# Performance work log

Hardware: AMD Instinct MI355X
Metric: run time of the kernel (lower is better)

The kernel has to match this reference:

```python
import jax, jax.numpy as jnp
import numpy as np


def setup_inputs() -> dict:
    key = jax.random.key(0)
    k1, k2, k3 = jax.random.split(key, 3)
    B, H, W, D, K = 16, 32, 32, 128, 32
    x = jax.random.normal(k1, (B, H, W, D), dtype=jnp.float32)
    std = 1.0 / (K * D) ** 0.5
    codewords = jax.random.uniform(k2, (K, D), minval=-std, maxval=std, dtype=jnp.float32)
    scale = jax.random.uniform(k3, (K,), minval=-1.0, maxval=0.0, dtype=jnp.float32)
    return {"x": x, "codewords": codewords, "scale": scale}


def reference(x, codewords, scale):
    B, H, W, D = x.shape
    K = codewords.shape[0]
    X = x.reshape(B, H * W, D)                      # [B, N, D]
    # scaled squared distances: s_k * ||x_n - c_k||^2 via expansion (no BNKD tensor)
    x2 = jnp.sum(X * X, axis=-1, keepdims=True)     # [B, N, 1]
    c2 = jnp.sum(codewords * codewords, axis=-1)    # [K]
    xc = jnp.einsum('bnd,kd->bnk', X, codewords)    # [B, N, K]
    SL = scale[None, None, :] * (x2 - 2.0 * xc + c2[None, None, :])
    A = jax.nn.softmax(SL, axis=2)                  # assignment weights [B, N, K]
    # E_bk = sum_n A_bnk * (x_bn - c_k)
    E = jnp.einsum('bnk,bnd->bkd', A, X) - jnp.sum(A, axis=1)[:, :, None] * codewords[None]
    return E
```

## Files before the change

kernel.cpp:

```cpp
#include <hip/hip_runtime.h>


typedef __attribute__((ext_vector_type(8))) short bf16x8;
typedef __attribute__((ext_vector_type(16))) float f32x16;

constexpr int XBS = 136;
constexpr int AST = 72;

__device__ __forceinline__ unsigned short f2bf(float f) {
    unsigned u = __float_as_uint(f);
    u += 0x7fffu + ((u >> 16) & 1u);
    return (unsigned short)(u >> 16);
}
__device__ __forceinline__ float bf2f(unsigned short h) {
    return __uint_as_float((unsigned)h << 16);
}

__global__ __launch_bounds__(256)
void enc_partial(const float* __restrict__ x, const float* __restrict__ cw,
                 const float* __restrict__ scale, unsigned short* __restrict__ ws)
{
    __shared__ unsigned short xb_s[64 * XBS];
    __shared__ unsigned short cb_s[32 * XBS];
    __shared__ unsigned short At_s[32 * AST];
    __shared__ float x2_s[64], c2_s[32];
    __shared__ float asum_s[4 * 32];
    __shared__ float asumf_s[32];

    const int tid = threadIdx.x;
    const int b   = blockIdx.x >> 4;
    const int s   = blockIdx.x & 15;
    const int lc  = tid & 31;
    const int lh  = (tid >> 5) & 1;
    const int w   = tid >> 6;
    const int g   = w >> 1;
    const int p   = w & 1;

    const float4* xg4 = (const float4*)(x + (size_t)(b * 1024 + s * 64) * 128);
    const float4* cg4 = (const float4*)cw;

#pragma unroll
    for (int i = 0; i < 8; ++i) {
        const int f   = tid + 256 * i;
        const int row = 8 * i + (tid >> 5);
        const int col = tid & 31;
        float4 vx = xg4[f];
        short4 hx = { (short)f2bf(vx.x), (short)f2bf(vx.y),
                      (short)f2bf(vx.z), (short)f2bf(vx.w) };
        *(short4*)&xb_s[row * XBS + col * 4] = hx;
        float sx = vx.x * vx.x + vx.y * vx.y + vx.z * vx.z + vx.w * vx.w;
#pragma unroll
        for (int m = 16; m >= 1; m >>= 1) sx += __shfl_xor(sx, m);
        if (col == 0) x2_s[row] = sx;
    }
#pragma unroll
    for (int i = 0; i < 4; ++i) {
        const int f   = tid + 256 * i;
        const int row = 8 * i + (tid >> 5);
        const int col = tid & 31;
        float4 vc = cg4[f];
        short4 hc = { (short)f2bf(vc.x), (short)f2bf(vc.y),
                      (short)f2bf(vc.z), (short)f2bf(vc.w) };
        *(short4*)&cb_s[row * XBS + col * 4] = hc;
        float sc = vc.x * vc.x + vc.y * vc.y + vc.z * vc.z + vc.w * vc.w;
#pragma unroll
        for (int m = 16; m >= 1; m >>= 1) sc += __shfl_xor(sc, m);
        if (col == 0) c2_s[row] = sc;
    }
    __syncthreads();

    f32x16 acc;
#pragma unroll
    for (int i = 0; i < 16; ++i) acc[i] = 0.f;
#pragma unroll
    for (int t = 0; t < 8; ++t) {
        bf16x8 af  = *(const bf16x8*)&xb_s[(32 * g + lc) * XBS + t * 16 + lh * 8];
        bf16x8 bfr = *(const bf16x8*)&cb_s[lc * XBS + t * 16 + lh * 8];
        acc = __builtin_amdgcn_mfma_f32_32x32x16_bf16(af, bfr, acc, 0, 0, 0);
    }

    {
        const float sck = scale[lc];
        const float c2k = c2_s[lc];
        float asum8 = 0.f;
#pragma unroll
        for (int j = 0; j < 2; ++j) {
            const int nb = 32 * g + 16 * p + 8 * j + 4 * lh;
            const float4 x2v = *(const float4*)&x2_s[nb];
            const int rb = 8 * p + 4 * j;
            float sl[4] = {
                sck * (x2v.x - 2.f * acc[rb + 0] + c2k),
                sck * (x2v.y - 2.f * acc[rb + 1] + c2k),
                sck * (x2v.z - 2.f * acc[rb + 2] + c2k),
                sck * (x2v.w - 2.f * acc[rb + 3] + c2k) };
            float a[4];
#pragma unroll
            for (int q = 0; q < 4; ++q) {
                float m = sl[q];
#pragma unroll
                for (int msk = 16; msk >= 1; msk >>= 1) m = fmaxf(m, __shfl_xor(m, msk));
                float e = __expf(sl[q] - m);
                float den = e;
#pragma unroll
                for (int msk = 16; msk >= 1; msk >>= 1) den += __shfl_xor(den, msk);
                a[q] = e / den;
            }
            short4 ha = { (short)f2bf(a[0]), (short)f2bf(a[1]),
                          (short)f2bf(a[2]), (short)f2bf(a[3]) };
            *(short4*)&At_s[lc * AST + nb] = ha;
            asum8 += (a[0] + a[1]) + (a[2] + a[3]);
        }
        asum8 += __shfl_xor(asum8, 32);
        if (lh == 0) asum_s[w * 32 + lc] = asum8;
    }
    __syncthreads();

    if (tid < 32)
        asumf_s[tid] = (asum_s[tid] + asum_s[32 + tid]) +
                       (asum_s[64 + tid] + asum_s[96 + tid]);

    f32x16 e;
#pragma unroll
    for (int i = 0; i < 16; ++i) e[i] = 0.f;
#pragma unroll
    for (int t = 0; t < 4; ++t) {
        bf16x8 af = *(const bf16x8*)&At_s[lc * AST + t * 16 + lh * 8];
        const int nb = t * 16 + lh * 8;
        bf16x8 bfr;
#pragma unroll
        for (int j = 0; j < 8; ++j)
            bfr[j] = (short)xb_s[(nb + j) * XBS + w * 32 + lc];
        e = __builtin_amdgcn_mfma_f32_32x32x16_bf16(af, bfr, e, 0, 0, 0);
    }
    __syncthreads();

    {
        unsigned short* wb = ws + (size_t)(b * 16 + s) * 4096;
        const int dd = w * 32 + lc;
#pragma unroll
        for (int r = 0; r < 16; ++r) {
            const int kk = (r & 3) + 8 * (r >> 2) + 4 * lh;
            float v = e[r] - asumf_s[kk] * bf2f(cb_s[kk * XBS + dd]);
            wb[kk * 128 + dd] = f2bf(v);
        }
    }
}

__global__ __launch_bounds__(256)
void enc_reduce(const unsigned short* __restrict__ ws, float* __restrict__ out)
{
    __shared__ float red_s[3][256];

    const int tid  = threadIdx.x;
    const int lane = tid & 63;
    const int sg   = tid >> 6;
    const int b    = blockIdx.x >> 4;
    const int q    = (blockIdx.x & 15) * 64 + lane;
    const unsigned short* base = ws + (size_t)b * 65536 + q * 4;

    float4 a0 = {0,0,0,0}, a1 = {0,0,0,0};
#pragma unroll
    for (int s = 0; s < 4; s += 2) {
        ushort4 v0 = *(const ushort4*)&base[(sg * 4 + s + 0) * 4096];
        ushort4 v1 = *(const ushort4*)&base[(sg * 4 + s + 1) * 4096];
        a0.x += bf2f(v0.x); a0.y += bf2f(v0.y); a0.z += bf2f(v0.z); a0.w += bf2f(v0.w);
        a1.x += bf2f(v1.x); a1.y += bf2f(v1.y); a1.z += bf2f(v1.z); a1.w += bf2f(v1.w);
    }
    float4 a;
    a.x = a0.x + a1.x; a.y = a0.y + a1.y; a.z = a0.z + a1.z; a.w = a0.w + a1.w;

    if (sg) *(float4*)&red_s[sg - 1][lane * 4] = a;
    __syncthreads();
    if (sg == 0) {
        float4 r0 = *(const float4*)&red_s[0][lane * 4];
        float4 r1 = *(const float4*)&red_s[1][lane * 4];
        float4 r2 = *(const float4*)&red_s[2][lane * 4];
        float4 r;
        r.x = (a.x + r0.x) + (r1.x + r2.x);
        r.y = (a.y + r0.y) + (r1.y + r2.y);
        r.z = (a.z + r0.z) + (r1.z + r2.z);
        r.w = (a.w + r0.w) + (r1.w + r2.w);
        *(float4*)&out[(size_t)b * 4096 + q * 4] = r;
    }
}

extern "C" void kernel_launch(void* const* d_in, const int* in_sizes, int n_in,
                              void* d_out, int out_size, void* d_ws, size_t ws_size,
                              hipStream_t stream)
{
    const float* x     = (const float*)d_in[0];
    const float* cw    = (const float*)d_in[1];
    const float* scale = (const float*)d_in[2];
    float* out = (float*)d_out;
    unsigned short* ws = (unsigned short*)d_ws;

    enc_partial<<<256, 256, 0, stream>>>(x, cw, scale, ws);
    enc_reduce<<<256, 256, 0, stream>>>(ws, out);
}
```

Measured before the change: 69.48 us.

## Double threads per block and split the N reduction across wave groups

Raises enc_partial to 512 threads (8 waves). Each wave computes softmax for a smaller slice of points, and the second MFMA stage is split by point half across two wave groups. The two partial results are then merged through a new fp32 shared buffer before the single bf16 write. This aims to raise parallelism and latency hiding in the small-grid kernel. In exchange it uses more LDS per block and adds a synchronisation and merge step. The reduce kernel's loop is manually unrolled.

```diff
diff --git a/kernel.cpp b/kernel.cpp
--- a/kernel.cpp
+++ b/kernel.cpp
@@ -5,7 +5,7 @@
 typedef __attribute__((ext_vector_type(16))) float f32x16;
 
 constexpr int XBS = 136;
-constexpr int AST = 72;
+constexpr int AST = 40;
 
 __device__ __forceinline__ unsigned short f2bf(float f) {
     unsigned u = __float_as_uint(f);
@@ -16,15 +16,16 @@
     return __uint_as_float((unsigned)h << 16);
 }
 
-__global__ __launch_bounds__(256)
+__global__ __launch_bounds__(512)
 void enc_partial(const float* __restrict__ x, const float* __restrict__ cw,
                  const float* __restrict__ scale, unsigned short* __restrict__ ws)
 {
     __shared__ unsigned short xb_s[64 * XBS];
     __shared__ unsigned short cb_s[32 * XBS];
-    __shared__ unsigned short At_s[32 * AST];
+    __shared__ unsigned short At_s[2 * 32 * AST];
+    __shared__ float merge_s[32 * 128];
     __shared__ float x2_s[64], c2_s[32];
-    __shared__ float asum_s[4 * 32];
+    __shared__ float asum_s[8 * 32];
     __shared__ float asumf_s[32];
 
     const int tid = threadIdx.x;
@@ -33,16 +34,16 @@
     const int lc  = tid & 31;
     const int lh  = (tid >> 5) & 1;
     const int w   = tid >> 6;
-    const int g   = w >> 1;
-    const int p   = w & 1;
+    const int g   = w >> 2;
+    const int wq  = w & 3;
 
     const float4* xg4 = (const float4*)(x + (size_t)(b * 1024 + s * 64) * 128);
     const float4* cg4 = (const float4*)cw;
 
 #pragma unroll
-    for (int i = 0; i < 8; ++i) {
-        const int f   = tid + 256 * i;
-        const int row = 8 * i + (tid >> 5);
+    for (int i = 0; i < 4; ++i) {
+        const int f   = tid + 512 * i;
+        const int row = 16 * i + (tid >> 5);
         const int col = tid & 31;
         float4 vx = xg4[f];
         short4 hx = { (short)f2bf(vx.x), (short)f2bf(vx.y),
@@ -54,9 +55,9 @@
         if (col == 0) x2_s[row] = sx;
     }
 #pragma unroll
-    for (int i = 0; i < 4; ++i) {
-        const int f   = tid + 256 * i;
-        const int row = 8 * i + (tid >> 5);
+    for (int i = 0; i < 2; ++i) {
+        const int f   = tid + 512 * i;
+        const int row = 16 * i + (tid >> 5);
         const int col = tid & 31;
         float4 vc = cg4[f];
         short4 hc = { (short)f2bf(vc.x), (short)f2bf(vc.y),
@@ -82,65 +83,73 @@
     {
         const float sck = scale[lc];
         const float c2k = c2_s[lc];
-        float asum8 = 0.f;
-#pragma unroll
-        for (int j = 0; j < 2; ++j) {
-            const int nb = 32 * g + 16 * p + 8 * j + 4 * lh;
-            const float4 x2v = *(const float4*)&x2_s[nb];
-            const int rb = 8 * p + 4 * j;
-            float sl[4] = {
-                sck * (x2v.x - 2.f * acc[rb + 0] + c2k),
-                sck * (x2v.y - 2.f * acc[rb + 1] + c2k),
-                sck * (x2v.z - 2.f * acc[rb + 2] + c2k),
-                sck * (x2v.w - 2.f * acc[rb + 3] + c2k) };
-            float a[4];
-#pragma unroll
-            for (int q = 0; q < 4; ++q) {
-                float m = sl[q];
-#pragma unroll
-                for (int msk = 16; msk >= 1; msk >>= 1) m = fmaxf(m, __shfl_xor(m, msk));
-                float e = __expf(sl[q] - m);
-                float den = e;
-#pragma unroll
-                for (int msk = 16; msk >= 1; msk >>= 1) den += __shfl_xor(den, msk);
-                a[q] = e / den;
-            }
-            short4 ha = { (short)f2bf(a[0]), (short)f2bf(a[1]),
-                          (short)f2bf(a[2]), (short)f2bf(a[3]) };
-            *(short4*)&At_s[lc * AST + nb] = ha;
-            asum8 += (a[0] + a[1]) + (a[2] + a[3]);
+        const float4 x2v = *(const float4*)&x2_s[32 * g + 8 * wq + 4 * lh];
+        float sl[4] = {
+            sck * (x2v.x - 2.f * acc[4 * wq + 0] + c2k),
+            sck * (x2v.y - 2.f * acc[4 * wq + 1] + c2k),
+            sck * (x2v.z - 2.f * acc[4 * wq + 2] + c2k),
+            sck * (x2v.w - 2.f * acc[4 * wq + 3] + c2k) };
+        float a[4];
+#pragma unroll
+        for (int q = 0; q < 4; ++q) {
+            float m = sl[q];
+#pragma unroll
+            for (int msk = 16; msk >= 1; msk >>= 1) m = fmaxf(m, __shfl_xor(m, msk));
+            float e = __expf(sl[q] - m);
+            float den = e;
+#pragma unroll
+            for (int msk = 16; msk >= 1; msk >>= 1) den += __shfl_xor(den, msk);
+            a[q] = e / den;
         }
-        asum8 += __shfl_xor(asum8, 32);
-        if (lh == 0) asum_s[w * 32 + lc] = asum8;
-    }
-    __syncthreads();
-
-    if (tid < 32)
-        asumf_s[tid] = (asum_s[tid] + asum_s[32 + tid]) +
-                       (asum_s[64 + tid] + asum_s[96 + tid]);
+        short4 ha = { (short)f2bf(a[0]), (short)f2bf(a[1]),
+                      (short)f2bf(a[2]), (short)f2bf(a[3]) };
+        *(short4*)&At_s[g * 32 * AST + lc * AST + 8 * wq + 4 * lh] = ha;
+        float ap = (a[0] + a[1]) + (a[2] + a[3]);
+        ap += __shfl_xor(ap, 32);
+        if (lh == 0) asum_s[w * 32 + lc] = ap;
+    }
+    __syncthreads();
+
+    if (tid < 32) {
+        float t0 = (asum_s[tid]       + asum_s[32 + tid]) +
+                   (asum_s[64 + tid]  + asum_s[96 + tid]);
+        float t1 = (asum_s[128 + tid] + asum_s[160 + tid]) +
+                   (asum_s[192 + tid] + asum_s[224 + tid]);
+        asumf_s[tid] = t0 + t1;
+    }
 
     f32x16 e;
 #pragma unroll
     for (int i = 0; i < 16; ++i) e[i] = 0.f;
 #pragma unroll
-    for (int t = 0; t < 4; ++t) {
-        bf16x8 af = *(const bf16x8*)&At_s[lc * AST + t * 16 + lh * 8];
+    for (int t = 0; t < 2; ++t) {
+        bf16x8 af = *(const bf16x8*)&At_s[g * 32 * AST + lc * AST + t * 16 + lh * 8];
         const int nb = t * 16 + lh * 8;
         bf16x8 bfr;
 #pragma unroll
         for (int j = 0; j < 8; ++j)
-            bfr[j] = (short)xb_s[(nb + j) * XBS + w * 32 + lc];
+            bfr[j] = (short)xb_s[(32 * g + nb + j) * XBS + wq * 32 + lc];
         e = __builtin_amdgcn_mfma_f32_32x32x16_bf16(af, bfr, e, 0, 0, 0);
     }
     __syncthreads();
 
-    {
-        unsigned short* wb = ws + (size_t)(b * 16 + s) * 4096;
-        const int dd = w * 32 + lc;
+    const int dd = wq * 32 + lc;
+    if (g == 1) {
 #pragma unroll
         for (int r = 0; r < 16; ++r) {
             const int kk = (r & 3) + 8 * (r >> 2) + 4 * lh;
-            float v = e[r] - asumf_s[kk] * bf2f(cb_s[kk * XBS + dd]);
+            merge_s[kk * 128 + dd] = e[r];
+        }
+    }
+    __syncthreads();
+
+    if (g == 0) {
+        unsigned short* wb = ws + (size_t)(b * 16 + s) * 4096;
+#pragma unroll
+        for (int r = 0; r < 16; ++r) {
+            const int kk = (r & 3) + 8 * (r >> 2) + 4 * lh;
+            float v = (e[r] + merge_s[kk * 128 + dd])
+                      - asumf_s[kk] * bf2f(cb_s[kk * XBS + dd]);
             wb[kk * 128 + dd] = f2bf(v);
         }
     }
@@ -159,12 +168,15 @@
     const unsigned short* base = ws + (size_t)b * 65536 + q * 4;
 
     float4 a0 = {0,0,0,0}, a1 = {0,0,0,0};
-#pragma unroll
-    for (int s = 0; s < 4; s += 2) {
-        ushort4 v0 = *(const ushort4*)&base[(sg * 4 + s + 0) * 4096];
-        ushort4 v1 = *(const ushort4*)&base[(sg * 4 + s + 1) * 4096];
+    {
+        ushort4 v0 = *(const ushort4*)&base[(sg * 4 + 0) * 4096];
+        ushort4 v1 = *(const ushort4*)&base[(sg * 4 + 1) * 4096];
+        ushort4 v2 = *(const ushort4*)&base[(sg * 4 + 2) * 4096];
+        ushort4 v3 = *(const ushort4*)&base[(sg * 4 + 3) * 4096];
         a0.x += bf2f(v0.x); a0.y += bf2f(v0.y); a0.z += bf2f(v0.z); a0.w += bf2f(v0.w);
         a1.x += bf2f(v1.x); a1.y += bf2f(v1.y); a1.z += bf2f(v1.z); a1.w += bf2f(v1.w);
+        a0.x += bf2f(v2.x); a0.y += bf2f(v2.y); a0.z += bf2f(v2.z); a0.w += bf2f(v2.w);
+        a1.x += bf2f(v3.x); a1.y += bf2f(v3.y); a1.z += bf2f(v3.z); a1.w += bf2f(v3.w);
     }
     float4 a;
     a.x = a0.x + a1.x; a.y = a0.y + a1.y; a.z = a0.z + a1.z; a.w = a0.w + a1.w;
@@ -194,6 +206,6 @@
     float* out = (float*)d_out;
     unsigned short* ws = (unsigned short*)d_ws;
 
-    enc_partial<<<256, 256, 0, stream>>>(x, cw, scale, ws);
+    enc_partial<<<256, 512, 0, stream>>>(x, cw, scale, ws);
     enc_reduce<<<256, 256, 0, stream>>>(ws, out);
 }
```

Result: faster. 66.35 us (-4.5%).
